# Kernel tuning notes

Hardware: AMD Instinct MI355X
Metric: run time of the kernel (lower is better)

The kernel has to match this reference:

```python
import jax, jax.numpy as jnp
import numpy as np

RATE_CHOICE = np.array([32, 64, 96, 128, 160, 192, 224, 256], dtype=np.int32)
B, C, S = 8, 256, 2048
RATE_NUM = len(RATE_CHOICE)
MAX_R = int(RATE_CHOICE.max())  # == C, required by residual add


def setup_inputs() -> dict:
    key = jax.random.key(0)
    k1, k2, k3, k4 = jax.random.split(key, 4)
    x = jax.random.normal(k1, (B, C, S), dtype=jnp.float32)
    indexes = jax.random.randint(k2, (B * S,), 0, RATE_NUM, dtype=jnp.int64)
    # kaiming-normal-ish weight, uniform bias as in the torch init
    weight = jax.random.normal(k3, (RATE_NUM, C, MAX_R), dtype=jnp.float32) * (1.0 / np.sqrt(C))
    bound = 1.0 / np.sqrt(C)
    bias = jax.random.uniform(k4, (RATE_NUM, MAX_R), dtype=jnp.float32, minval=-bound, maxval=bound)
    rate_choice = jnp.asarray(RATE_CHOICE)
    return {"x": x, "indexes": indexes, "weight": weight, "bias": bias, "rate_choice": rate_choice}


def reference(x, indexes, weight, bias, rate_choice):
    b_, c_, s_ = x.shape
    max_r = weight.shape[-1]
    x_blc = jnp.transpose(x, (0, 2, 1))              # (B, S, C)
    idx = indexes.reshape(b_, s_).astype(jnp.int32)  # (B, S)
    # Dense per-expert GEMM then select expert per token (same math as
    # index_select(weight, indexes) followed by per-token matmul, but avoids
    # materializing the (B,S,C,maxR) gathered weight tensor).
    all_proj = jnp.einsum('bsc,rcm->bsrm', x_blc, weight)        # (B, S, R, maxR)
    proj = jnp.take_along_axis(all_proj, idx[:, :, None, None], axis=2)[:, :, 0, :]  # (B, S, maxR)
    btok = bias[idx]                                             # (B, S, maxR)
    rc = rate_choice[idx]                                        # (B, S)
    mask = (jnp.arange(max_r)[None, None, :] < rc[:, :, None]).astype(x.dtype)  # (B, S, maxR)
    y = (x_blc + proj + btok) * mask                             # (B, S, maxR); maxR == C
    x_masked = jnp.transpose(y, (0, 2, 1))       # (B, maxR, S)
    mask_bchw = jnp.transpose(mask, (0, 2, 1))   # (B, maxR, S)
    return x_masked, mask_bchw, indexes
```

## Files before the change

### kernel.cpp

```cpp
#include <hip/hip_runtime.h>

#define B_ 8
#define C_ 256
#define S_ 2048
#define T_ (B_*S_)

typedef short s8v __attribute__((ext_vector_type(8)));
typedef short s4v __attribute__((ext_vector_type(4)));
typedef float f4v __attribute__((ext_vector_type(4)));

__device__ inline short f2b(float f){
  unsigned u = __builtin_bit_cast(unsigned, f);
  unsigned r = (u + 0x7FFFu + ((u >> 16) & 1u)) >> 16;
  return (short)r;
}
__device__ inline float b2f(short s){
  unsigned u = ((unsigned)(unsigned short)s) << 16;
  return __builtin_bit_cast(float, u);
}

__global__ __launch_bounds__(256) void k_pre(const float* __restrict__ x, short* __restrict__ xT,
                                             const float* __restrict__ wgt, short* __restrict__ wT2,
                                             const int* __restrict__ idx, int* __restrict__ segCnt,
                                             int* __restrict__ segBucket, float* __restrict__ idx_out){
  __shared__ float tile[64][65];
  int tid = threadIdx.x;
  int bid = blockIdx.x;

  if (bid < 1024){
    int b  = bid >> 7;
    int ct = (bid >> 5) & 3;
    int st = bid & 31;
    const float* xb = x + b*(C_*S_);
    #pragma unroll
    for (int it = 0; it < 4; ++it){
      int row = it*16 + (tid >> 4);
      int s4  = tid & 15;
      float4 v = *(const float4*)(xb + (ct*64 + row)*S_ + st*64 + s4*4);
      tile[row][s4*4+0] = v.x; tile[row][s4*4+1] = v.y;
      tile[row][s4*4+2] = v.z; tile[row][s4*4+3] = v.w;
    }
    __syncthreads();
    #pragma unroll
    for (int it = 0; it < 4; ++it){
      int srow = it*16 + (tid >> 4);
      int c4   = tid & 15;
      s4v o;
      o[0] = f2b(tile[c4*4+0][srow]); o[1] = f2b(tile[c4*4+1][srow]);
      o[2] = f2b(tile[c4*4+2][srow]); o[3] = f2b(tile[c4*4+3][srow]);
      *(s4v*)(xT + (b*S_ + st*64 + srow)*C_ + ct*64 + c4*4) = o;
    }
  } else if (bid < 1152){
    int wb_ = bid - 1024;
    int r  = wb_ >> 4;
    int ct = (wb_ >> 2) & 3;
    int mt = wb_ & 3;
    const float* wsrc = wgt + r*(C_*256);
    #pragma unroll
    for (int it = 0; it < 4; ++it){
      int row = it*16 + (tid >> 4);
      int m4  = tid & 15;
      float4 v = *(const float4*)(wsrc + (ct*64 + row)*256 + mt*64 + m4*4);
      tile[row][m4*4+0] = v.x; tile[row][m4*4+1] = v.y;
      tile[row][m4*4+2] = v.z; tile[row][m4*4+3] = v.w;
    }
    __syncthreads();
    char* wdst = (char*)wT2 + r*131072;
    #pragma unroll
    for (int it = 0; it < 2; ++it){
      int q  = it*256 + tid;
      int ml = q >> 3;
      int ck = q & 7;
      int mg = mt*64 + ml;
      int cg = ct*64 + ck*8;
      int kcb = cg >> 5, klocal = cg & 31;
      s8v o;
      #pragma unroll
      for (int j = 0; j < 8; ++j) o[j] = f2b(tile[ck*8 + j][ml]);
      *(s8v*)(wdst + kcb*16384 + mg*64 + klocal*2) = o;
    }
  } else {
    int seg = bid - 1152;
    __shared__ int lcount[8];
    __shared__ int lbase[8];
    int t = seg*256 + tid;
    if (tid < 8) lcount[tid] = 0;
    __syncthreads();
    int ei = idx[t];
    int e  = ei & 7;
    int lp = atomicAdd(&lcount[e], 1);
    __syncthreads();
    if (tid == 0){
      int a0 = 0;
      #pragma unroll
      for (int e2 = 0; e2 < 8; ++e2){ lbase[e2] = a0; a0 += lcount[e2]; }
    }
    __syncthreads();
    if (tid < 8) segCnt[seg*8 + tid] = lcount[tid];
    segBucket[seg*256 + lbase[e] + lp] = t;
    idx_out[t] = (float)ei;
  }
}

__global__ __launch_bounds__(256,2) void k_gemm(const short* __restrict__ xT, const short* __restrict__ wT2,
                                                const float* __restrict__ bias, const int* __restrict__ segCnt,
                                                const int* __restrict__ segBucket, const int* __restrict__ rate,
                                                short* __restrict__ yT){
  int bid = blockIdx.x;
  int e   = bid & 7;
  int seg = bid >> 3;

  __shared__ short A [32*256];
  __shared__ short OS[32*256];
  __shared__ float biasS[256];
  __shared__ int   toks[32];

  int tid  = threadIdx.x;
  int lane = tid & 63, wv = tid >> 6;
  int l15  = lane & 15, lq = lane >> 4;

  biasS[tid] = bias[e*256 + tid];
  int rate_e = rate[e];

  int off = 0, cnt = 0;
  #pragma unroll
  for (int j = 0; j < 8; ++j){
    int c = segCnt[seg*8 + j];
    if (j < e) off += c;
    if (j == e) cnt = c;
  }
  const int* list = segBucket + seg*256 + off;

  const char* wTe = (const char*)wT2 + e*131072;
  char* AB  = (char*)A;
  char* OSB = (char*)OS;

  for (int t0 = 0; t0 < cnt; t0 += 32){
    int rowsV = cnt - t0; if (rowsV > 32) rowsV = 32;
    __syncthreads();
    if (tid < 32)
      toks[tid] = list[t0 + (tid < rowsV ? tid : rowsV - 1)];
    __syncthreads();

    {
      int row = tid >> 3, ck = tid & 7;
      const char* src = (const char*)xT + toks[row]*512 + ck*64;
      s8v v0 = *(const s8v*)(src);
      s8v v1 = *(const s8v*)(src + 16);
      s8v v2 = *(const s8v*)(src + 32);
      s8v v3 = *(const s8v*)(src + 48);
      int base = row*512, swz = (row & 7) << 4;
      *(s8v*)(AB + base + ((ck*64 +  0) ^ swz)) = v0;
      *(s8v*)(AB + base + ((ck*64 + 16) ^ swz)) = v1;
      *(s8v*)(AB + base + ((ck*64 + 32) ^ swz)) = v2;
      *(s8v*)(AB + base + ((ck*64 + 48) ^ swz)) = v3;
    }
    __syncthreads();

    f4v acc[2][4];
    #pragma unroll
    for (int mi = 0; mi < 2; ++mi)
      #pragma unroll
      for (int ni = 0; ni < 4; ++ni) acc[mi][ni] = (f4v){0.f,0.f,0.f,0.f};

    int aswz = (l15 & 7) << 4;
    #pragma unroll
    for (int kc = 0; kc < 8; ++kc){
      s8v a0 = *(const s8v*)(AB + l15*512        + ((kc*64 + lq*16) ^ aswz));
      s8v a1 = *(const s8v*)(AB + (16 + l15)*512 + ((kc*64 + lq*16) ^ aswz));
      #pragma unroll
      for (int ni = 0; ni < 4; ++ni){
        int n = wv*64 + ni*16 + l15;
        s8v bv = *(const s8v*)(wTe + kc*16384 + n*64 + lq*16);
        acc[0][ni] = __builtin_amdgcn_mfma_f32_16x16x32_bf16(a0, bv, acc[0][ni], 0, 0, 0);
        acc[1][ni] = __builtin_amdgcn_mfma_f32_16x16x32_bf16(a1, bv, acc[1][ni], 0, 0, 0);
      }
    }

    #pragma unroll
    for (int mi = 0; mi < 2; ++mi){
      #pragma unroll
      for (int ni = 0; ni < 4; ++ni){
        int col = wv*64 + ni*16 + l15;
        float bs = biasS[col];
        bool keep = col < rate_e;
        #pragma unroll
        for (int r = 0; r < 4; ++r){
          int row = mi*16 + lq*4 + r;
          float xres = b2f(*(const short*)(AB + row*512 + ((col*2) ^ ((row & 7) << 4))));
          float val  = keep ? (acc[mi][ni][r] + xres + bs) : 0.0f;
          *(short*)(OSB + row*512 + ((col*2) ^ ((row & 3) << 5))) = f2b(val);
        }
      }
    }
    __syncthreads();
    #pragma unroll
    for (int r2 = 0; r2 < 4; ++r2){
      int q = r2*4096 + tid*16;
      int row = q >> 9, off2 = q & 511;
      if (row < rowsV)
        *(s8v*)((char*)yT + toks[row]*512 + (off2 ^ ((row & 3) << 5))) = *(const s8v*)(OSB + q);
    }
  }
}

__global__ __launch_bounds__(256) void k_final(const short* __restrict__ yT, const int* __restrict__ idx,
                                               const int* __restrict__ rate_choice,
                                               float* __restrict__ outx, float* __restrict__ outm){
  int bid = blockIdx.x;
  int b  = bid >> 7;
  int ct = (bid >> 5) & 3;
  int st = bid & 31;
  __shared__ float tile[64][65];
  __shared__ int rateS[64];
  int tid = threadIdx.x;
  if (tid < 64) rateS[tid] = rate_choice[idx[b*S_ + st*64 + tid] & 7] >> 5;
  #pragma unroll
  for (int it = 0; it < 4; ++it){
    int srow = it*16 + (tid >> 4);
    int c4   = tid & 15;
    s4v v = *(const s4v*)(yT + (b*S_ + st*64 + srow)*C_ + ct*64 + c4*4);
    tile[c4*4+0][srow] = b2f(v[0]); tile[c4*4+1][srow] = b2f(v[1]);
    tile[c4*4+2][srow] = b2f(v[2]); tile[c4*4+3][srow] = b2f(v[3]);
  }
  __syncthreads();
  #pragma unroll
  for (int it = 0; it < 16; ++it){
    int cl = it*4 + (tid >> 6);
    int sl = tid & 63;
    int cg = ct*64 + cl;
    float v = tile[cl][sl];
    bool keep = (cg >> 5) < rateS[sl];
    int off = b*(C_*S_) + cg*S_ + st*64 + sl;
    outx[off] = v;
    outm[off] = keep ? 1.0f : 0.0f;
  }
}

extern "C" void kernel_launch(void* const* d_in, const int* in_sizes, int n_in,
                              void* d_out, int out_size, void* d_ws, size_t ws_size,
                              hipStream_t stream){
  const float* x    = (const float*)d_in[0];
  const int*   idx  = (const int*)d_in[1];
  const float* wgt  = (const float*)d_in[2];
  const float* bias = (const float*)d_in[3];
  const int*   rate = (const int*)d_in[4];

  char* ws = (char*)d_ws;
  short* xT        = (short*)ws;
  short* wT2       = (short*)(ws + 8388608);
  int*   segBucket = (int*)  (ws + 9437184);
  int*   segCnt    = (int*)  (ws + 9502720);
  short* yT        = (short*)(ws + 10485760);

  float* outx    = (float*)d_out;
  float* outm    = outx + (B_*C_*S_);
  float* idx_out = outx + 2*(B_*C_*S_);

  k_pre  <<<1216, 256, 0, stream>>>(x, xT, wgt, wT2, idx, segCnt, segBucket, idx_out);
  k_gemm <<<512,  256, 0, stream>>>(xT, wT2, bias, segCnt, segBucket, rate, yT);
  k_final<<<1024, 256, 0, stream>>>(yT, idx, rate, outx, outm);
}
```

Before: 35.29 us.

## Fuse expert GEMM with transpose/output kernel via 128-token segments

Merges the GEMM and final transpose kernels into one. Each block takes a 128-token segment sorted by expert plus a 64-column slice of the output. It stages token rows into LDS with asynchronous global-to-LDS loads into a double buffer, and runs MFMAs over every expert present in each 16-row group, keeping the result for the matching expert. The transposed tile is written straight to the fp32 outputs and mask, which removes the bf16 yT intermediate round-trip and one launch. In exchange, groups that mix experts do redundant MFMA work, and each block reloads weights for its column slice.

```diff
diff --git a/kernel.cpp b/kernel.cpp
--- a/kernel.cpp
+++ b/kernel.cpp
@@ -17,6 +17,12 @@
 __device__ inline float b2f(short s){
   unsigned u = ((unsigned)(unsigned short)s) << 16;
   return __builtin_bit_cast(float, u);
+}
+
+__device__ inline void glds16(const void* g, void* l){
+  __builtin_amdgcn_global_load_lds(
+      (const __attribute__((address_space(1))) unsigned int*)g,
+      (__attribute__((address_space(3))) unsigned int*)l, 16, 0, 0);
 }
 
 __global__ __launch_bounds__(256) void k_pre(const float* __restrict__ x, short* __restrict__ xT,
@@ -80,160 +86,163 @@
       *(s8v*)(wdst + kcb*16384 + mg*64 + klocal*2) = o;
     }
   } else {
-    int seg = bid - 1152;
-    __shared__ int lcount[8];
-    __shared__ int lbase[8];
-    int t = seg*256 + tid;
-    if (tid < 8) lcount[tid] = 0;
-    __syncthreads();
+    int blk = bid - 1152;
+    __shared__ int lcount[2][8], lbase2[2][8];
+    int h  = tid >> 7;
+    int lt = tid & 127;
+    int seg = blk*2 + h;
+    if (lt < 8) lcount[h][lt] = 0;
+    __syncthreads();
+    int t  = seg*128 + lt;
     int ei = idx[t];
     int e  = ei & 7;
-    int lp = atomicAdd(&lcount[e], 1);
-    __syncthreads();
-    if (tid == 0){
+    int lp = atomicAdd(&lcount[h][e], 1);
+    __syncthreads();
+    if (lt == 0){
       int a0 = 0;
       #pragma unroll
-      for (int e2 = 0; e2 < 8; ++e2){ lbase[e2] = a0; a0 += lcount[e2]; }
-    }
-    __syncthreads();
-    if (tid < 8) segCnt[seg*8 + tid] = lcount[tid];
-    segBucket[seg*256 + lbase[e] + lp] = t;
+      for (int e2 = 0; e2 < 8; ++e2){ lbase2[h][e2] = a0; a0 += lcount[h][e2]; }
+    }
+    __syncthreads();
+    if (lt < 8) segCnt[seg*8 + lt] = lcount[h][lt];
+    segBucket[seg*128 + lbase2[h][e] + lp] = t;
     idx_out[t] = (float)ei;
   }
 }
 
-__global__ __launch_bounds__(256,2) void k_gemm(const short* __restrict__ xT, const short* __restrict__ wT2,
+__global__ __launch_bounds__(256,2) void k_main(const short* __restrict__ xT, const short* __restrict__ wT2,
                                                 const float* __restrict__ bias, const int* __restrict__ segCnt,
                                                 const int* __restrict__ segBucket, const int* __restrict__ rate,
-                                                short* __restrict__ yT){
+                                                float* __restrict__ outx, float* __restrict__ outm){
   int bid = blockIdx.x;
-  int e   = bid & 7;
-  int seg = bid >> 3;
-
-  __shared__ short A [32*256];
-  __shared__ short OS[32*256];
-  __shared__ float biasS[256];
-  __shared__ int   toks[32];
-
-  int tid  = threadIdx.x;
-  int lane = tid & 63, wv = tid >> 6;
-  int l15  = lane & 15, lq = lane >> 4;
-
-  biasS[tid] = bias[e*256 + tid];
-  int rate_e = rate[e];
-
-  int off = 0, cnt = 0;
-  #pragma unroll
-  for (int j = 0; j < 8; ++j){
-    int c = segCnt[seg*8 + j];
-    if (j < e) off += c;
-    if (j == e) cnt = c;
-  }
-  const int* list = segBucket + seg*256 + off;
-
-  const char* wTe = (const char*)wT2 + e*131072;
-  char* AB  = (char*)A;
-  char* OSB = (char*)OS;
-
-  for (int t0 = 0; t0 < cnt; t0 += 32){
-    int rowsV = cnt - t0; if (rowsV > 32) rowsV = 32;
-    __syncthreads();
-    if (tid < 32)
-      toks[tid] = list[t0 + (tid < rowsV ? tid : rowsV - 1)];
-    __syncthreads();
-
-    {
-      int row = tid >> 3, ck = tid & 7;
-      const char* src = (const char*)xT + toks[row]*512 + ck*64;
-      s8v v0 = *(const s8v*)(src);
-      s8v v1 = *(const s8v*)(src + 16);
-      s8v v2 = *(const s8v*)(src + 32);
-      s8v v3 = *(const s8v*)(src + 48);
-      int base = row*512, swz = (row & 7) << 4;
-      *(s8v*)(AB + base + ((ck*64 +  0) ^ swz)) = v0;
-      *(s8v*)(AB + base + ((ck*64 + 16) ^ swz)) = v1;
-      *(s8v*)(AB + base + ((ck*64 + 32) ^ swz)) = v2;
-      *(s8v*)(AB + base + ((ck*64 + 48) ^ swz)) = v3;
-    }
-    __syncthreads();
-
-    f4v acc[2][4];
-    #pragma unroll
-    for (int mi = 0; mi < 2; ++mi)
-      #pragma unroll
-      for (int ni = 0; ni < 4; ++ni) acc[mi][ni] = (f4v){0.f,0.f,0.f,0.f};
-
+  int q   = (bid >> 3) & 3;
+  int seg = (bid & 7) | ((bid >> 5) << 3);
+  int b   = seg >> 4;
+  int s0  = (seg & 15) << 7;
+
+  __shared__ short A[2][32*256];
+  __shared__ short OS[64*136];
+  __shared__ float biasQ[8*64];
+  __shared__ int slocal8[128];
+  __shared__ int eSlot[128];
+  __shared__ int maskR[128];
+  __shared__ int eRangeG[8];
+  __shared__ int rateE[8];
+  __shared__ int cum[9];
+
+  int tid = threadIdx.x, lane = tid & 63, wv = tid >> 6;
+  int l15 = lane & 15, lq = lane >> 4;
+
+  if (tid < 8) rateE[tid] = rate[tid];
+  { int e = tid >> 5, j = (tid & 31)*2;
+    float2 bv2 = *(const float2*)(bias + e*256 + q*64 + j);
+    biasQ[e*64 + j] = bv2.x; biasQ[e*64 + j + 1] = bv2.y; }
+  if (tid == 0){
+    int a0 = 0; cum[0] = 0;
+    #pragma unroll
+    for (int e2 = 0; e2 < 8; ++e2){ a0 += segCnt[seg*8 + e2]; cum[e2+1] = a0; }
+  }
+  __syncthreads();
+  if (tid < 128){
+    int t  = segBucket[seg*128 + tid];
+    int sl = t & 127;
+    int e  = 0;
+    #pragma unroll
+    for (int j = 1; j < 8; ++j) e += (tid >= cum[j]);
+    slocal8[tid] = sl;
+    eSlot[tid]   = e;
+    maskR[sl]    = rateE[e] >> 5;
+  }
+  __syncthreads();
+  if (tid < 8) eRangeG[tid] = eSlot[tid*16] | (eSlot[tid*16 + 15] << 8);
+
+  const char* xTb = (const char*)xT;
+  auto STAGE = [&](int bufi, int sub){
+    #pragma unroll
+    for (int j = 0; j < 4; ++j){
+      int base = wv*4096 + j*1024;
+      int row  = wv*8 + j*2 + (lane >> 5);
+      int tok  = seg*128 + slocal8[sub*32 + row];
+      int off  = (lane & 31)*16;
+      glds16(xTb + tok*512 + (off ^ ((row & 7) << 4)), (char*)A[bufi] + base);
+    }
+  };
+
+  STAGE(0, 0);
+  int cur = 0;
+  int cg  = q*64 + wv*16 + l15;
+  float bsE[8];
+  (void)bsE;
+
+  for (int sub = 0; sub < 4; ++sub){
+    __syncthreads();
+    if (sub < 3) STAGE(cur ^ 1, sub + 1);
+
+    const char* ABc = (const char*)A[cur];
+    s8v aF[2][8];
     int aswz = (l15 & 7) << 4;
     #pragma unroll
     for (int kc = 0; kc < 8; ++kc){
-      s8v a0 = *(const s8v*)(AB + l15*512        + ((kc*64 + lq*16) ^ aswz));
-      s8v a1 = *(const s8v*)(AB + (16 + l15)*512 + ((kc*64 + lq*16) ^ aswz));
-      #pragma unroll
-      for (int ni = 0; ni < 4; ++ni){
-        int n = wv*64 + ni*16 + l15;
-        s8v bv = *(const s8v*)(wTe + kc*16384 + n*64 + lq*16);
-        acc[0][ni] = __builtin_amdgcn_mfma_f32_16x16x32_bf16(a0, bv, acc[0][ni], 0, 0, 0);
-        acc[1][ni] = __builtin_amdgcn_mfma_f32_16x16x32_bf16(a1, bv, acc[1][ni], 0, 0, 0);
-      }
+      aF[0][kc] = *(const s8v*)(ABc + l15*512        + ((kc*64 + lq*16) ^ aswz));
+      aF[1][kc] = *(const s8v*)(ABc + (16 + l15)*512 + ((kc*64 + lq*16) ^ aswz));
     }
 
     #pragma unroll
     for (int mi = 0; mi < 2; ++mi){
-      #pragma unroll
-      for (int ni = 0; ni < 4; ++ni){
-        int col = wv*64 + ni*16 + l15;
-        float bs = biasS[col];
-        bool keep = col < rate_e;
+      int g  = sub*2 + mi;
+      int rg = eRangeG[g], elo = rg & 255, ehi = rg >> 8;
+      int qb = sub*32 + mi*16 + lq*4;
+      int epk = eSlot[qb] | (eSlot[qb+1] << 8) | (eSlot[qb+2] << 16) | (eSlot[qb+3] << 24);
+      f4v acc = (f4v){0.f,0.f,0.f,0.f};
+      for (int e = elo; e <= ehi; ++e){
+        const char* bp = (const char*)wT2 + e*131072 + cg*64 + lq*16;
+        f4v t = (f4v){0.f,0.f,0.f,0.f};
+        #pragma unroll
+        for (int kc = 0; kc < 8; ++kc){
+          s8v bv = *(const s8v*)(bp + kc*16384);
+          t = __builtin_amdgcn_mfma_f32_16x16x32_bf16(aF[mi][kc], bv, t, 0, 0, 0);
+        }
+        float bs = biasQ[e*64 + wv*16 + l15];
         #pragma unroll
         for (int r = 0; r < 4; ++r){
-          int row = mi*16 + lq*4 + r;
-          float xres = b2f(*(const short*)(AB + row*512 + ((col*2) ^ ((row & 7) << 4))));
-          float val  = keep ? (acc[mi][ni][r] + xres + bs) : 0.0f;
-          *(short*)(OSB + row*512 + ((col*2) ^ ((row & 3) << 5))) = f2b(val);
+          bool hit = (((epk >> (r*8)) & 255) == e);
+          acc[r] = hit ? (t[r] + bs) : acc[r];
         }
       }
-    }
-    __syncthreads();
-    #pragma unroll
-    for (int r2 = 0; r2 < 4; ++r2){
-      int q = r2*4096 + tid*16;
-      int row = q >> 9, off2 = q & 511;
-      if (row < rowsV)
-        *(s8v*)((char*)yT + toks[row]*512 + (off2 ^ ((row & 3) << 5))) = *(const s8v*)(OSB + q);
-    }
-  }
-}
-
-__global__ __launch_bounds__(256) void k_final(const short* __restrict__ yT, const int* __restrict__ idx,
-                                               const int* __restrict__ rate_choice,
-                                               float* __restrict__ outx, float* __restrict__ outm){
-  int bid = blockIdx.x;
-  int b  = bid >> 7;
-  int ct = (bid >> 5) & 3;
-  int st = bid & 31;
-  __shared__ float tile[64][65];
-  __shared__ int rateS[64];
-  int tid = threadIdx.x;
-  if (tid < 64) rateS[tid] = rate_choice[idx[b*S_ + st*64 + tid] & 7] >> 5;
-  #pragma unroll
-  for (int it = 0; it < 4; ++it){
-    int srow = it*16 + (tid >> 4);
-    int c4   = tid & 15;
-    s4v v = *(const s4v*)(yT + (b*S_ + st*64 + srow)*C_ + ct*64 + c4*4);
-    tile[c4*4+0][srow] = b2f(v[0]); tile[c4*4+1][srow] = b2f(v[1]);
-    tile[c4*4+2][srow] = b2f(v[2]); tile[c4*4+3][srow] = b2f(v[3]);
+      #pragma unroll
+      for (int r = 0; r < 4; ++r){
+        int rowL = mi*16 + lq*4 + r;
+        int sl   = slocal8[sub*32 + rowL];
+        int er   = (epk >> (r*8)) & 255;
+        float xres = b2f(*(const short*)(ABc + rowL*512 + ((cg*2) ^ ((rowL & 7) << 4))));
+        float val  = (cg < rateE[er]) ? (acc[r] + xres) : 0.0f;
+        OS[(wv*16 + l15)*136 + sl] = f2b(val);
+      }
+    }
+    cur ^= 1;
   }
   __syncthreads();
-  #pragma unroll
-  for (int it = 0; it < 16; ++it){
-    int cl = it*4 + (tid >> 6);
-    int sl = tid & 63;
-    int cg = ct*64 + cl;
-    float v = tile[cl][sl];
-    bool keep = (cg >> 5) < rateS[sl];
-    int off = b*(C_*S_) + cg*S_ + st*64 + sl;
-    outx[off] = v;
-    outm[off] = keep ? 1.0f : 0.0f;
+
+  {
+    float* ob = outx + b*(C_*S_) + s0;
+    float* om = outm + b*(C_*S_) + s0;
+    #pragma unroll
+    for (int it = 0; it < 8; ++it){
+      int q2 = it*256 + tid;
+      int cl = q2 >> 5;
+      int s4 = (q2 & 31)*4;
+      s4v v = *(const s4v*)((const char*)OS + cl*272 + s4*2);
+      int cgl = q*64 + cl;
+      int mk  = cgl >> 5;
+      float4 ov, mv;
+      ov.x = b2f(v[0]); ov.y = b2f(v[1]); ov.z = b2f(v[2]); ov.w = b2f(v[3]);
+      mv.x = (mk < maskR[s4+0]) ? 1.0f : 0.0f;
+      mv.y = (mk < maskR[s4+1]) ? 1.0f : 0.0f;
+      mv.z = (mk < maskR[s4+2]) ? 1.0f : 0.0f;
+      mv.w = (mk < maskR[s4+3]) ? 1.0f : 0.0f;
+      *(float4*)(ob + cgl*S_ + s4) = ov;
+      *(float4*)(om + cgl*S_ + s4) = mv;
+    }
   }
 }
 
@@ -251,13 +260,11 @@
   short* wT2       = (short*)(ws + 8388608);
   int*   segBucket = (int*)  (ws + 9437184);
   int*   segCnt    = (int*)  (ws + 9502720);
-  short* yT        = (short*)(ws + 10485760);
 
   float* outx    = (float*)d_out;
   float* outm    = outx + (B_*C_*S_);
   float* idx_out = outx + 2*(B_*C_*S_);
 
-  k_pre  <<<1216, 256, 0, stream>>>(x, xT, wgt, wT2, idx, segCnt, segBucket, idx_out);
-  k_gemm <<<512,  256, 0, stream>>>(xT, wT2, bias, segCnt, segBucket, rate, yT);
-  k_final<<<1024, 256, 0, stream>>>(yT, idx, rate, outx, outm);
-}
+  k_pre <<<1216, 256, 0, stream>>>(x, xT, wgt, wT2, idx, segCnt, segBucket, idx_out);
+  k_main<<<512,  256, 0, stream>>>(xT, wT2, bias, segCnt, segBucket, rate, outx, outm);
+}
```

Result: slower. 37.36 us (+5.9%).
